# Optimization experiments

Measured on AMD Instinct MI355X. Metric: run time of the kernel, lower is better.

## Reference

```python
import jax, jax.numpy as jnp
import numpy as np

H, DK, NHID, L, G = 8, 32, 256, 2, 16
SQRT_DK = float(np.sqrt(DK))
N_IN = (3, 3, 2)  # number of etypes whose dst is word, topic, doc (for mean cross-reducer)


def _seg_softmax_agg(a, val, dst, n):
    # per-destination-node softmax over incoming edges (DGL mailbox softmax), then weighted sum
    m = jax.ops.segment_max(a, dst, num_segments=n)
    m = jnp.where(m < -1e30, 0.0, m)  # empty segments
    ex = jnp.exp(a - m[dst])
    den = jax.ops.segment_sum(ex, dst, num_segments=n)
    w = ex / jnp.maximum(den, 1e-9)[dst]
    return jax.ops.segment_sum(w[..., None] * val, dst, num_segments=n)  # [n,H,DK]


def _forward(word_id, topic_id, g_word, g_topic, g_doc,
             src_ww, dst_ww, src_wd, dst_wd, src_wt, dst_wt, src_td, dst_td, src_tt, dst_tt,
             time_ww, time_wd, time_wt, time_td, y_data,
             word_embeds, topic_embeds, doc_gen, adapt_w, adapt_b,
             time_tab, time_w, time_b,
             kW, kB, qW, qB, vW, vB, aW, aB, skip, ln_g, ln_b,
             pri, attR, msgR, out_w, out_b):
    nd = g_doc.shape[0]
    # initial node features: word via adapt_ws, topic lookup, doc broadcast
    h = [word_embeds[word_id] @ adapt_w + adapt_b,
         topic_embeds[topic_id],
         jnp.tile(doc_gen, (nd, 1))]
    te = lambda t: time_tab[t] @ time_w + time_b  # RelTemporalEncoding: lin(emb(t)) -> [E, DK]
    th_ww, th_wd, th_wt, th_td = te(time_ww), te(time_wd), te(time_wt), te(time_td)
    # etype index order: wt, wd, td, tt, ww, tw, dt, dw ; ntype index: 0=word,1=topic,2=doc
    rels = [(0, 0, 1, src_wt, dst_wt, th_wt), (1, 0, 2, src_wd, dst_wd, th_wd),
            (2, 1, 2, src_td, dst_td, th_td), (3, 1, 1, src_tt, dst_tt, None),
            (4, 0, 0, src_ww, dst_ww, th_ww), (5, 1, 0, dst_wt, src_wt, th_wt),
            (6, 2, 1, dst_td, src_td, th_td), (7, 2, 0, dst_wd, src_wd, th_wd)]
    for li in range(L):
        k = [(h[i] @ kW[li, i] + kB[li, i]).reshape(-1, H, DK) for i in range(3)]
        q = [(h[i] @ qW[li, i] + qB[li, i]).reshape(-1, H, DK) for i in range(3)]
        v = [(h[i] @ vW[li, i] + vB[li, i]).reshape(-1, H, DK) for i in range(3)]
        t = [jnp.zeros((h[i].shape[0], NHID), h[i].dtype) for i in range(3)]
        for (e, s, d, src, dst, th) in rels:
            key = jnp.einsum('ehk,hkl->ehl', k[s][src], attR[li, e])
            a = (q[d][dst] * key).sum(-1) * pri[li, e] / SQRT_DK  # [E,H]
            val = jnp.einsum('ehk,hkl->ehl', v[s][src], msgR[li, e])
            if th is not None:
                val = val + th[:, None, :]  # temporal encoding broadcast over heads
            n = h[d].shape[0]
            he = _seg_softmax_agg(a, val, dst, n)
            t[d] = t[d] + jax.nn.relu(he.reshape(n, NHID))  # relu per etype, then mean
        nh = []
        for i in range(3):
            alpha = jax.nn.sigmoid(skip[li, i])
            trans = (t[i] / N_IN[i]) @ aW[li, i] + aB[li, i]
            out = trans * alpha + h[i] * (1.0 - alpha)
            mu = out.mean(-1, keepdims=True)
            var = ((out - mu) ** 2).mean(-1, keepdims=True)
            nh.append((out - mu) / jnp.sqrt(var + 1e-5) * ln_g[li, i] + ln_b[li, i])
        h = nh
    gmax = lambda x, g: jax.ops.segment_max(x, g, num_segments=G)  # dgl.max_nodes
    gi = jnp.concatenate([gmax(h[2], g_doc), gmax(h[0], g_word), gmax(h[1], g_topic)], -1)
    logits = gi @ out_w + out_b  # [G,1]
    z = logits.reshape(-1)
    loss = jnp.mean(jnp.maximum(z, 0.0) - z * y_data + jnp.log1p(jnp.exp(-jnp.abs(z))))
    return loss, jax.nn.sigmoid(logits)


def setup_inputs():
    key = jax.random.key(0)
    ks = iter(jax.random.split(key, 80))
    nrm = lambda shape, s=0.05: jax.random.normal(next(ks), shape, jnp.float32) * s
    ri = lambda shape, hi: jax.random.randint(next(ks), shape, 0, hi)
    NW, NT, ND = 30000, 2000, 8000
    d = {}
    d['word_id'] = ri((NW,), 15000)
    d['topic_id'] = ri((NT,), 50)
    d['g_word'] = jnp.sort(ri((NW,), G))
    d['g_topic'] = jnp.sort(ri((NT,), G))
    d['g_doc'] = jnp.sort(ri((ND,), G))
    d['src_ww'] = ri((40000,), NW); d['dst_ww'] = ri((40000,), NW); d['time_ww'] = ri((40000,), 7)
    d['src_wd'] = ri((30000,), NW); d['dst_wd'] = ri((30000,), ND); d['time_wd'] = ri((30000,), 7)
    d['src_wt'] = ri((30000,), NW); d['dst_wt'] = ri((30000,), NT); d['time_wt'] = ri((30000,), 7)
    d['src_td'] = ri((25000,), NT); d['dst_td'] = ri((25000,), ND); d['time_td'] = ri((25000,), 7)
    d['src_tt'] = ri((20000,), NT); d['dst_tt'] = ri((20000,), NT)
    d['y_data'] = jax.random.uniform(next(ks), (G,), jnp.float32)
    d['word_embeds'] = nrm((15000, 256))
    d['topic_embeds'] = nrm((50, 256), 0.1)
    d['doc_gen'] = nrm((1, 256), 0.1)
    d['adapt_w'] = nrm((256, 256)); d['adapt_b'] = nrm((256,), 0.01)
    d['time_tab'] = nrm((7, 32), 0.1); d['time_w'] = nrm((32, 32), 0.1); d['time_b'] = nrm((32,), 0.01)
    for nm in ['kW', 'qW', 'vW', 'aW']:
        d[nm] = nrm((L, 3, 256, 256))
    for nm in ['kB', 'qB', 'vB', 'aB']:
        d[nm] = nrm((L, 3, 256), 0.01)
    d['skip'] = jnp.ones((L, 3))
    d['ln_g'] = jnp.ones((L, 3, 256)); d['ln_b'] = jnp.zeros((L, 3, 256))
    d['pri'] = jnp.ones((L, 8, H))
    d['attR'] = nrm((L, 8, H, DK, DK), 0.1)
    d['msgR'] = nrm((L, 8, H, DK, DK), 0.1)
    d['out_w'] = nrm((3 * NHID, 1)); d['out_b'] = jnp.zeros((1,))
    return d


def reference(word_id, topic_id, g_word, g_topic, g_doc,
              src_ww, dst_ww, time_ww, src_wd, dst_wd, time_wd,
              src_wt, dst_wt, time_wt, src_td, dst_td, time_td,
              src_tt, dst_tt, y_data,
              word_embeds, topic_embeds, doc_gen, adapt_w, adapt_b,
              time_tab, time_w, time_b,
              kW, kB, qW, qB, vW, vB, aW, aB, skip, ln_g, ln_b,
              pri, attR, msgR, out_w, out_b):
    return _forward(word_id, topic_id, g_word, g_topic, g_doc,
                    src_ww, dst_ww, src_wd, dst_wd, src_wt, dst_wt, src_td, dst_td, src_tt, dst_tt,
                    time_ww, time_wd, time_wt, time_td, y_data,
                    word_embeds, topic_embeds, doc_gen, adapt_w, adapt_b,
                    time_tab, time_w, time_b,
                    kW, kB, qW, qB, vW, vB, aW, aB, skip, ln_g, ln_b,
                    pri, attR, msgR, out_w, out_b)
```

## Files before the change

kernel.cpp:

```cpp
#include <hip/hip_runtime.h>
#include <hip/hip_bf16.h>
#include <math.h>

#define H 8
#define DK 32
#define NHID 256
#define LNUM 2
#define GNUM 16

typedef float f32x4 __attribute__((ext_vector_type(4)));
typedef short bf16x8 __attribute__((ext_vector_type(8)));
typedef unsigned short u16x8 __attribute__((ext_vector_type(8)));

__device__ __forceinline__ unsigned encf(float f) {
    unsigned u = __float_as_uint(f);
    return (u & 0x80000000u) ? ~u : (u | 0x80000000u);
}
__device__ __forceinline__ float decf(unsigned u) {
    return __uint_as_float((u & 0x80000000u) ? (u ^ 0x80000000u) : ~u);
}
__device__ __forceinline__ float bfd(unsigned short u) {
    return __uint_as_float(((unsigned)u) << 16);
}
__device__ __forceinline__ unsigned short f2bf(float x) {
    __hip_bfloat16 b = __float2bfloat16(x);
    return *reinterpret_cast<unsigned short*>(&b);
}

#define APAN2(row, kb) ((((kb) >> 7) << 12) + ((row) << 6) + ((((kb) & 127) ^ (((row) & 7) << 4)) >> 1))
__device__ __forceinline__ size_t swzA(int row, int col ) {
    return (((size_t)(row >> 6)) << 14) + (size_t)APAN2(row & 63, col * 2);
}
#define SWZB(row, kb)  (((row) << 6) + ((((kb) ^ (((row) & 7) << 4))) >> 1))

struct CsrArgs { const int* dst[8]; int relOfs[9]; int dstBase[8]; };
struct BdArgs  { const unsigned short* inK[3]; const unsigned short* inV[3];
                 const float* RA[3]; const float* RM[3]; const float* priP[3];
                 int rows[3]; int rowOfs[3]; };
struct Ek1Args { const int* src[3]; const int* dst[3]; int E[3]; int eBase[3]; int rowOfs[3]; };
struct Ek3Args { const int* src[3]; const int* tim[3]; int eBase[3]; int dstBase[3];
                 int rowOfs[3]; int nr; int nD; };
struct GmaxArgs{ const float* hp[3]; const int* grp[3]; int n[3]; int colBase[3]; };
struct GBArgs  { int rb[4]; int nLoc[3]; int li3; };
struct MLArgs  { int rowOfs[4]; int nLoc[3]; int li3; };

__global__ void te_kernel(const float* __restrict__ time_tab, const float* __restrict__ time_w,
                          const float* __restrict__ time_b, float* __restrict__ te7) {
    int t = threadIdx.x >> 5, j = threadIdx.x & 31;
    if (t < 7) {
        float s = time_b[j];
        #pragma unroll
        for (int i = 0; i < 32; ++i) s += time_tab[t * 32 + i] * time_w[i * 32 + j];
        te7[t * 32 + j] = s;
    }
}

__global__ void gather_rows(const float* __restrict__ emb, const int* __restrict__ idx,
                            float* __restrict__ out, unsigned short* __restrict__ outB, int n) {
    int row = blockIdx.x, c = threadIdx.x;
    if (row < n) {
        float v = emb[(size_t)idx[row] * 256 + c];
        out[(size_t)row * 256 + c] = v;
        outB[swzA(row, c)] = f2bf(v);
    }
}

__global__ void bcast_row(const float* __restrict__ src, float* __restrict__ out,
                          unsigned short* __restrict__ outB, int n) {
    int row = blockIdx.x, c = threadIdx.x;
    if (row < n) {
        float v = src[c];
        out[(size_t)row * 256 + c] = v;
        outB[swzA(row, c)] = f2bf(v);
    }
}

__global__ __launch_bounds__(256) void wtr_kernel(
    const float* __restrict__ adaptW, const float* __restrict__ kW, const float* __restrict__ qW,
    const float* __restrict__ vW, const float* __restrict__ aW, unsigned short* __restrict__ WT) {
    int z = blockIdx.z;
    const float* src;
    if (z == 0) src = adaptW;
    else if (z < 7)  src = kW + (size_t)(z - 1) * 65536;
    else if (z < 13) src = qW + (size_t)(z - 7) * 65536;
    else if (z < 19) src = vW + (size_t)(z - 13) * 65536;
    else             src = aW + (size_t)(z - 19) * 65536;
    unsigned short* dst = WT + (size_t)z * 65536;
    __shared__ float tile[32][33];
    int tx = threadIdx.x & 31, ty = threadIdx.x >> 5;
    int kb = blockIdx.x * 32, cb = blockIdx.y * 32;
    #pragma unroll
    for (int i = 0; i < 4; ++i)
        tile[ty + i * 8][tx] = src[(size_t)(kb + ty + i * 8) * 256 + cb + tx];
    __syncthreads();
    #pragma unroll
    for (int i = 0; i < 4; ++i)
        dst[(size_t)(cb + ty + i * 8) * 256 + kb + tx] = f2bf(tile[tx][ty + i * 8]);
}

__global__ __launch_bounds__(256) void gemm_batch(
    const unsigned short* __restrict__ Apan,
    const unsigned short* __restrict__ WT, int wBase, int nz,
    const float* __restrict__ b0, const float* __restrict__ b1, const float* __restrict__ b2,
    void* __restrict__ o0, void* __restrict__ o1, void* __restrict__ o2,
    int outBf16, GBArgs ga)
{
    __shared__ unsigned short As[64 * 256];
    __shared__ unsigned short Bs[2][64 * 64];
    const int tid = threadIdx.x;
    const int lane = tid & 63, wv = tid >> 6;
    const int b = blockIdx.x;
    const int t = (b >= ga.rb[2]) ? 2 : ((b >= ga.rb[1]) ? 1 : 0);
    const int nLoc = ga.nLoc[t];
    const int locRowBase = (b - ga.rb[t]) * 64;
    const int cb = blockIdx.y * 64;
    const int mBase = wBase + ga.li3 + t;
    {
        const u16x8* src = reinterpret_cast<const u16x8*>(Apan + (((size_t)b) << 14));
        u16x8* dst = reinterpret_cast<u16x8*>(As);
        #pragma unroll
        for (int it = 0; it < 8; ++it)
            dst[it * 256 + tid] = src[it * 256 + tid];
    }
    const int fr = lane & 15, fg = lane >> 4;
    const int wrow = (wv & 1) * 32, wcol = (wv >> 1) * 32;
    const int bcol = tid >> 2, bseg = tid & 3;
    const int nt = nz * 4;
    {
        const unsigned short* bsrc = WT + (size_t)mBase * 65536 + (size_t)(cb + bcol) * 256 + bseg * 16;
        u16x8 w0 = *reinterpret_cast<const u16x8*>(bsrc);
        u16x8 w1 = *reinterpret_cast<const u16x8*>(bsrc + 8);
        *reinterpret_cast<u16x8*>(&Bs[0][SWZB(bcol, bseg * 32)])      = w0;
        *reinterpret_cast<u16x8*>(&Bs[0][SWZB(bcol, bseg * 32 + 16)]) = w1;
    }
    __syncthreads();

    f32x4 acc[2][2];
    #pragma unroll
    for (int m = 0; m < 2; ++m)
        #pragma unroll
        for (int nn = 0; nn < 2; ++nn) acc[m][nn] = 0.f;

    for (int tt2 = 0; tt2 < nt; ++tt2) {
        const int cur = tt2 & 1;
        const int ks = tt2 & 3, z = tt2 >> 2;
        u16x8 w0, w1;
        const bool pf = (tt2 + 1 < nt);
        if (pf) {
            int tn = tt2 + 1;
            const unsigned short* bsrc = WT + (size_t)(mBase + (tn >> 2) * 6) * 65536
                                            + (size_t)(cb + bcol) * 256 + (tn & 3) * 64 + bseg * 16;
            w0 = *reinterpret_cast<const u16x8*>(bsrc);
            w1 = *reinterpret_cast<const u16x8*>(bsrc + 8);
        }
        #pragma unroll
        for (int kk = 0; kk < 2; ++kk) {
            bf16x8 af0 = *reinterpret_cast<bf16x8*>(&As[APAN2(wrow + fr,      ks * 128 + kk * 64 + fg * 16)]);
            bf16x8 af1 = *reinterpret_cast<bf16x8*>(&As[APAN2(wrow + 16 + fr, ks * 128 + kk * 64 + fg * 16)]);
            bf16x8 bf0 = *reinterpret_cast<bf16x8*>(&Bs[cur][SWZB(wcol + fr,      kk * 64 + fg * 16)]);
            bf16x8 bf1 = *reinterpret_cast<bf16x8*>(&Bs[cur][SWZB(wcol + 16 + fr, kk * 64 + fg * 16)]);
            acc[0][0] = __builtin_amdgcn_mfma_f32_16x16x32_bf16(af0, bf0, acc[0][0], 0, 0, 0);
            acc[0][1] = __builtin_amdgcn_mfma_f32_16x16x32_bf16(af0, bf1, acc[0][1], 0, 0, 0);
            acc[1][0] = __builtin_amdgcn_mfma_f32_16x16x32_bf16(af1, bf0, acc[1][0], 0, 0, 0);
            acc[1][1] = __builtin_amdgcn_mfma_f32_16x16x32_bf16(af1, bf1, acc[1][1], 0, 0, 0);
        }
        if (pf) {
            *reinterpret_cast<u16x8*>(&Bs[cur ^ 1][SWZB(bcol, bseg * 32)])      = w0;
            *reinterpret_cast<u16x8*>(&Bs[cur ^ 1][SWZB(bcol, bseg * 32 + 16)]) = w1;
        }
        if (ks == 3) {
            const float* biasB = (z == 0) ? b0 : ((z == 1) ? b1 : b2);
            const float* bias = biasB + (size_t)(ga.li3 + t) * 256;
            void* outp = (z == 0) ? o0 : ((z == 1) ? o1 : o2);
            #pragma unroll
            for (int m = 0; m < 2; ++m) {
                #pragma unroll
                for (int r = 0; r < 4; ++r) {
                    int lr = locRowBase + wrow + m * 16 + fg * 4 + r;
                    if (lr >= nLoc) continue;
                    size_t gr = (size_t)b * 64 + wrow + m * 16 + fg * 4 + r;
                    #pragma unroll
                    for (int nn = 0; nn < 2; ++nn) {
                        int gc = cb + wcol + nn * 16 + fr;
                        float v = acc[m][nn][r] + bias[gc];
                        if (outBf16) ((unsigned short*)outp)[gr * 256 + gc] = f2bf(v);
                        else         ((float*)outp)[gr * 256 + gc] = v;
                    }
                }
            }
            #pragma unroll
            for (int m = 0; m < 2; ++m)
                #pragma unroll
                for (int nn = 0; nn < 2; ++nn) acc[m][nn] = 0.f;
        }
        __syncthreads();
    }
}

__global__ __launch_bounds__(256) void gemm_init(
    const float* __restrict__ A, const int* __restrict__ gidx,
    const unsigned short* __restrict__ WT, const float* __restrict__ bias,
    float* __restrict__ outF, unsigned short* __restrict__ dupB, int n)
{
    __shared__ unsigned short As[64 * 256];
    __shared__ unsigned short Bs[2][64 * 64];
    const int tid = threadIdx.x;
    const int lane = tid & 63, wv = tid >> 6;
    const int rowBase = blockIdx.x * 64;
    const int cb = blockIdx.y * 64;
    #pragma unroll 4
    for (int it = 0; it < 16; ++it) {
        int row = it * 4 + wv;
        int r = rowBase + row;
        ushort4 p = make_ushort4(0, 0, 0, 0);
        if (r < n) {
            int ar = gidx[r];
            float4 v = *reinterpret_cast<const float4*>(A + (size_t)ar * 256 + lane * 4);
            p.x = f2bf(v.x); p.y = f2bf(v.y); p.z = f2bf(v.z); p.w = f2bf(v.w);
        }
        *reinterpret_cast<ushort4*>(&As[APAN2(row, lane * 8)]) = p;
    }
    const int fr = lane & 15, fg = lane >> 4;
    const int wrow = (wv & 1) * 32, wcol = (wv >> 1) * 32;
    const int bcol = tid >> 2, bseg = tid & 3;
    {
        const unsigned short* bsrc = WT + (size_t)(cb + bcol) * 256 + bseg * 16;
        u16x8 w0 = *reinterpret_cast<const u16x8*>(bsrc);
        u16x8 w1 = *reinterpret_cast<const u16x8*>(bsrc + 8);
        *reinterpret_cast<u16x8*>(&Bs[0][SWZB(bcol, bseg * 32)])      = w0;
        *reinterpret_cast<u16x8*>(&Bs[0][SWZB(bcol, bseg * 32 + 16)]) = w1;
    }
    __syncthreads();
    f32x4 acc[2][2];
    #pragma unroll
    for (int m = 0; m < 2; ++m)
        #pragma unroll
        for (int nn = 0; nn < 2; ++nn) acc[m][nn] = 0.f;
    for (int t = 0; t < 4; ++t) {
        const int cur = t & 1;
        u16x8 w0, w1;
        const bool pf = (t + 1 < 4);
        if (pf) {
            const unsigned short* bsrc = WT + (size_t)(cb + bcol) * 256 + (t + 1) * 64 + bseg * 16;
            w0 = *reinterpret_cast<const u16x8*>(bsrc);
            w1 = *reinterpret_cast<const u16x8*>(bsrc + 8);
        }
        #pragma unroll
        for (int kk = 0; kk < 2; ++kk) {
            bf16x8 af0 = *reinterpret_cast<bf16x8*>(&As[APAN2(wrow + fr,      t * 128 + kk * 64 + fg * 16)]);
            bf16x8 af1 = *reinterpret_cast<bf16x8*>(&As[APAN2(wrow + 16 + fr, t * 128 + kk * 64 + fg * 16)]);
            bf16x8 bf0 = *reinterpret_cast<bf16x8*>(&Bs[cur][SWZB(wcol + fr,      kk * 64 + fg * 16)]);
            bf16x8 bf1 = *reinterpret_cast<bf16x8*>(&Bs[cur][SWZB(wcol + 16 + fr, kk * 64 + fg * 16)]);
            acc[0][0] = __builtin_amdgcn_mfma_f32_16x16x32_bf16(af0, bf0, acc[0][0], 0, 0, 0);
            acc[0][1] = __builtin_amdgcn_mfma_f32_16x16x32_bf16(af0, bf1, acc[0][1], 0, 0, 0);
            acc[1][0] = __builtin_amdgcn_mfma_f32_16x16x32_bf16(af1, bf0, acc[1][0], 0, 0, 0);
            acc[1][1] = __builtin_amdgcn_mfma_f32_16x16x32_bf16(af1, bf1, acc[1][1], 0, 0, 0);
        }
        if (pf) {
            *reinterpret_cast<u16x8*>(&Bs[cur ^ 1][SWZB(bcol, bseg * 32)])      = w0;
            *reinterpret_cast<u16x8*>(&Bs[cur ^ 1][SWZB(bcol, bseg * 32 + 16)]) = w1;
        }
        __syncthreads();
    }
    #pragma unroll
    for (int m = 0; m < 2; ++m) {
        #pragma unroll
        for (int r = 0; r < 4; ++r) {
            int gr = rowBase + wrow + m * 16 + fg * 4 + r;
            if (gr >= n) continue;
            #pragma unroll
            for (int nn = 0; nn < 2; ++nn) {
                int gc = cb + wcol + nn * 16 + fr;
                float v = acc[m][nn][r] + bias[gc];
                outF[(size_t)gr * 256 + gc] = v;
                dupB[swzA(gr, gc)] = f2bf(v);
            }
        }
    }
}

__global__ __launch_bounds__(256) void bd_mfma(
    unsigned short* __restrict__ katt, unsigned short* __restrict__ vmsg, BdArgs A)
{
    const int rr = blockIdx.z >> 1, isV = blockIdx.z & 1;
    const int n = A.rows[rr];
    const int rowBase = blockIdx.x * 128;
    if (rowBase >= n) return;
    const unsigned short* in = isV ? A.inV[rr] : A.inK[rr];
    const float* R = isV ? A.RM[rr] : A.RA[rr];
    unsigned short* out = (isV ? vmsg : katt) + (size_t)A.rowOfs[rr] * 256;
    const int head = blockIdx.y;
    const float oscale = isV ? 1.f : (A.priP[rr][head] * 0.17677669529663687f);
    const int tid = threadIdx.x, lane = tid & 63, wv = tid >> 6;
    const int fr = lane & 15, fg = lane >> 4;
    const float* Rh = R + head * 1024;
    bf16x8 b0, b1;
    #pragma unroll
    for (int j = 0; j < 8; ++j) {
        b0[j] = (short)f2bf(Rh[(fg * 8 + j) * 32 + fr] * oscale);
        b1[j] = (short)f2bf(Rh[(fg * 8 + j) * 32 + 16 + fr] * oscale);
    }
    const int r0 = rowBase + wv * 32 + fr;
    const int r1 = r0 + 16;
    const int rc0 = (r0 < n) ? r0 : n - 1;
    const int rc1 = (r1 < n) ? r1 : n - 1;
    bf16x8 a0 = *reinterpret_cast<const bf16x8*>(in + (size_t)rc0 * 256 + head * 32 + fg * 8);
    bf16x8 a1 = *reinterpret_cast<const bf16x8*>(in + (size_t)rc1 * 256 + head * 32 + fg * 8);
    f32x4 acc00 = 0.f, acc01 = 0.f, acc10 = 0.f, acc11 = 0.f;
    acc00 = __builtin_amdgcn_mfma_f32_16x16x32_bf16(a0, b0, acc00, 0, 0, 0);
    acc01 = __builtin_amdgcn_mfma_f32_16x16x32_bf16(a0, b1, acc01, 0, 0, 0);
    acc10 = __builtin_amdgcn_mfma_f32_16x16x32_bf16(a1, b0, acc10, 0, 0, 0);
    acc11 = __builtin_amdgcn_mfma_f32_16x16x32_bf16(a1, b1, acc11, 0, 0, 0);
    const int colB = head * 32 + fr;
    #pragma unroll
    for (int r = 0; r < 4; ++r) {
        int g0 = rowBase + wv * 32 + fg * 4 + r;
        if (g0 < n) {
            out[(size_t)g0 * 256 + colB]      = f2bf(acc00[r]);
            out[(size_t)g0 * 256 + colB + 16] = f2bf(acc01[r]);
        }
        int g1 = g0 + 16;
        if (g1 < n) {
            out[(size_t)g1 * 256 + colB]      = f2bf(acc10[r]);
            out[(size_t)g1 * 256 + colB + 16] = f2bf(acc11[r]);
        }
    }
}

__global__ __launch_bounds__(256) void ek1_group(
    const unsigned short* __restrict__ qbuf, const unsigned short* __restrict__ katt,
    float* __restrict__ alog, Ek1Args A)
{
    const int rr = blockIdx.y;
    int gid = blockIdx.x * 256 + threadIdx.x;
    int e = gid >> 3, h = gid & 7;
    if (e >= A.E[rr]) return;
    int s = A.src[rr][e], d = A.dst[rr][e];
    const u16x8* q8 = reinterpret_cast<const u16x8*>(qbuf + (size_t)d * 256 + h * 32);
    const u16x8* k8 = reinterpret_cast<const u16x8*>(katt + ((size_t)(A.rowOfs[rr] + s)) * 256 + h * 32);
    float a = 0.f;
    #pragma unroll
    for (int j = 0; j < 4; ++j) {
        u16x8 qv = q8[j], kv = k8[j];
        #pragma unroll
        for (int m = 0; m < 8; ++m) a += bfd(qv[m]) * bfd(kv[m]);
    }
    alog[(size_t)(A.eBase[rr] + e) * 8 + h] = a;
}

__global__ __launch_bounds__(256) void ek3_group(
    const unsigned short* __restrict__ vmsg, const float* __restrict__ alog,
    const int* __restrict__ rowptrAll, const int* __restrict__ eidxAll,
    const float* __restrict__ te7, unsigned short* __restrict__ tacc, float outScale, Ek3Args A)
{
    __shared__ float sTe[224];
    if (threadIdx.x < 224) sTe[threadIdx.x] = te7[threadIdx.x];
    __syncthreads();
    int wv = threadIdx.x >> 6, lane = threadIdx.x & 63;
    int d = blockIdx.x * 4 + wv;
    if (d >= A.nD) return;
    const int bl = lane >> 3, hl = lane & 7;
    const int c = lane * 4, hq = lane >> 3;
    float t0 = 0.f, t1 = 0.f, t2 = 0.f, t3 = 0.f;
    for (int rr = 0; rr < A.nr; ++rr) {
        int base = A.dstBase[rr] + d;
        int beg = rowptrAll[base], end = rowptrAll[base + 1];
        if (beg == end) continue;
        const int* srcp = A.src[rr];
        const int* timp = A.tim[rr];
        int eB = A.eBase[rr], rO = A.rowOfs[rr];
        float m = -INFINITY, den = 0.f;
        float a0 = 0.f, a1 = 0.f, a2 = 0.f, a3 = 0.f;
        for (int p0 = beg; p0 < end; p0 += 8) {
            int p = p0 + bl;
            bool valid = p < end;
            int ge = eidxAll[valid ? p : end - 1];
            int le = ge - eB;
            float a = valid ? alog[(size_t)ge * 8 + hl] : -INFINITY;
            int sS = valid ? srcp[le] : 0;
            int tT = (timp && valid) ? timp[le] : 0;
            float bm = a;
            bm = fmaxf(bm, __shfl_xor(bm, 8));
            bm = fmaxf(bm, __shfl_xor(bm, 16));
            bm = fmaxf(bm, __shfl_xor(bm, 32));
            float bmA = __shfl(bm, hq);
            float mN = fmaxf(m, bmA);
            float sc = __expf(m - mN);
            den *= sc; a0 *= sc; a1 *= sc; a2 *= sc; a3 *= sc;
            m = mN;
            float mL = __shfl(mN, hl * 8);
            float ex = valid ? __expf(a - mL) : 0.f;
            float ds = ex;
            ds += __shfl_xor(ds, 8);
            ds += __shfl_xor(ds, 16);
            ds += __shfl_xor(ds, 32);
            den += __shfl(ds, hq);
            int nb = end - p0; if (nb > 8) nb = 8;
            for (int b = 0; b < nb; ++b) {
                float w = __shfl(ex, b * 8 + hq);
                int sB = __shfl(sS, b * 8);
                ushort4 v = *reinterpret_cast<const ushort4*>(vmsg + ((size_t)(rO + sB)) * 256 + c);
                float vx = bfd(v.x), vy = bfd(v.y), vz = bfd(v.z), vw = bfd(v.w);
                if (timp) {
                    int tB = __shfl(tT, b * 8);
                    const float* tp = &sTe[tB * 32 + (c & 31)];
                    vx += tp[0]; vy += tp[1]; vz += tp[2]; vw += tp[3];
                }
                a0 += w * vx; a1 += w * vy; a2 += w * vz; a3 += w * vw;
            }
        }
        float inv = 1.f / fmaxf(den, 1e-9f);
        t0 += fmaxf(a0 * inv, 0.f); t1 += fmaxf(a1 * inv, 0.f);
        t2 += fmaxf(a2 * inv, 0.f); t3 += fmaxf(a3 * inv, 0.f);
    }
    ushort4 o;
    o.x = f2bf(t0 * outScale); o.y = f2bf(t1 * outScale);
    o.z = f2bf(t2 * outScale); o.w = f2bf(t3 * outScale);
    *reinterpret_cast<ushort4*>(tacc + swzA(d, c)) = o;
}

__global__ void count_all(CsrArgs A, int* __restrict__ cnt, int totE) {
    int gid = blockIdx.x * 256 + threadIdx.x;
    if (gid >= totE) return;
    int r = 0;
    while (gid >= A.relOfs[r + 1]) ++r;
    int e = gid - A.relOfs[r];
    atomicAdd(&cnt[A.dstBase[r] + A.dst[r][e]], 1);
}
__global__ __launch_bounds__(1024) void scan1_k(const int* __restrict__ cnt, int* __restrict__ part,
                                                int* __restrict__ bsum, int n) {
    __shared__ int buf[1024];
    int tid = threadIdx.x, gid = blockIdx.x * 1024 + tid;
    int x = (gid < n) ? cnt[gid] : 0;
    buf[tid] = x; __syncthreads();
    for (int off = 1; off < 1024; off <<= 1) {
        int y = (tid >= off) ? buf[tid - off] : 0;
        __syncthreads();
        buf[tid] += y;
        __syncthreads();
    }
    if (gid < n) part[gid] = buf[tid];
    if (tid == 1023) bsum[blockIdx.x] = buf[1023];
}
__global__ __launch_bounds__(256) void scan2_k(int* __restrict__ bsum, int nb) {
    __shared__ int buf[256];
    int tid = threadIdx.x;
    buf[tid] = (tid < nb) ? bsum[tid] : 0;
    __syncthreads();
    for (int off = 1; off < 256; off <<= 1) {
        int y = (tid >= off) ? buf[tid - off] : 0;
        __syncthreads();
        buf[tid] += y;
        __syncthreads();
    }
    if (tid < nb) bsum[tid] = buf[tid];
}
__global__ void scan3_k(const int* __restrict__ cnt, const int* __restrict__ part,
                        const int* __restrict__ bsum, int* __restrict__ rowptr,
                        int* __restrict__ cur, int n) {
    int gid = blockIdx.x * 256 + threadIdx.x;
    if (gid < n) {
        int b = gid >> 10;
        int add = (b > 0) ? bsum[b - 1] : 0;
        int inc = part[gid] + add;
        rowptr[gid + 1] = inc;
        cur[gid] = inc - cnt[gid];
    }
    if (gid == 0) rowptr[0] = 0;
}
__global__ void scatter_all(CsrArgs A, int* __restrict__ cur, int* __restrict__ eidx, int totE) {
    int gid = blockIdx.x * 256 + threadIdx.x;
    if (gid >= totE) return;
    int r = 0;
    while (gid >= A.relOfs[r + 1]) ++r;
    int e = gid - A.relOfs[r];
    int p = atomicAdd(&cur[A.dstBase[r] + A.dst[r][e]], 1);
    eidx[p] = gid;
}

__global__ __launch_bounds__(256) void mix_ln_all(
    float* __restrict__ h, unsigned short* __restrict__ hB, const float* __restrict__ trans,
    const float* __restrict__ skipP, const float* __restrict__ g, const float* __restrict__ b,
    MLArgs M)
{
    int row = blockIdx.x;
    int t = (row >= M.rowOfs[2]) ? 2 : ((row >= M.rowOfs[1]) ? 1 : 0);
    int d = row - M.rowOfs[t];
    if (d >= M.nLoc[t]) return;
    int j = M.li3 + t;
    int c = threadIdx.x;
    float alpha = 1.f / (1.f + expf(-skipP[j]));
    size_t off = (size_t)row * 256 + c;
    float o = trans[off] * alpha + h[off] * (1.f - alpha);
    float s = o, ss = o * o;
    #pragma unroll
    for (int dd = 1; dd < 64; dd <<= 1) { s += __shfl_xor(s, dd); ss += __shfl_xor(ss, dd); }
    __shared__ float rS[4], rSS[4];
    int w = threadIdx.x >> 6, lane = threadIdx.x & 63;
    if (lane == 0) { rS[w] = s; rSS[w] = ss; }
    __syncthreads();
    float S = rS[0] + rS[1] + rS[2] + rS[3];
    float SS = rSS[0] + rSS[1] + rSS[2] + rSS[3];
    float mean = S * (1.f / 256.f);
    float var = fmaxf(SS * (1.f / 256.f) - mean * mean, 0.f);
    float rs = rsqrtf(var + 1e-5f);
    float v = (o - mean) * rs * g[(size_t)j * 256 + c] + b[(size_t)j * 256 + c];
    h[off] = v;
    hB[swzA(row, c)] = f2bf(v);
}

__global__ __launch_bounds__(256) void gmax_all(GmaxArgs A, unsigned* __restrict__ gi) {
    int ty = blockIdx.y;
    int n = A.n[ty];
    int r0 = blockIdx.x * 64;
    if (r0 >= n) return;
    int col = threadIdx.x;
    const float* hp = A.hp[ty];
    const int* grp = A.grp[ty];
    int cbase = A.colBase[ty];
    int rend = (r0 + 64 < n) ? r0 + 64 : n;
    int cur = grp[r0];
    float m = -INFINITY;
    for (int r = r0; r < rend; ++r) {
        int g = grp[r];
        if (g != cur) {
            atomicMax(&gi[cur * 768 + cbase + col], encf(m));
            cur = g; m = -INFINITY;
        }
        m = fmaxf(m, hp[(size_t)r * 256 + col]);
    }
    atomicMax(&gi[cur * 768 + cbase + col], encf(m));
}

__global__ void gi_init(unsigned* __restrict__ gi) {
    int i = blockIdx.x * 256 + threadIdx.x;
    if (i < 16 * 768) gi[i] = 0x007FFFFFu;
}

__global__ __launch_bounds__(1024) void final_k(const unsigned* __restrict__ gi,
                                                const float* __restrict__ out_w,
                                                const float* __restrict__ out_b,
                                                const float* __restrict__ y,
                                                float* __restrict__ out) {
    int w = threadIdx.x >> 6, lane = threadIdx.x & 63;
    float s = 0.f;
    for (int c = lane; c < 768; c += 64) s += decf(gi[w * 768 + c]) * out_w[c];
    #pragma unroll
    for (int d = 1; d < 64; d <<= 1) s += __shfl_xor(s, d);
    __shared__ float lloss[16];
    if (lane == 0) {
        float z = s + out_b[0];
        out[1 + w] = 1.f / (1.f + expf(-z));
        lloss[w] = fmaxf(z, 0.f) - z * y[w] + log1pf(expf(-fabsf(z)));
    }
    __syncthreads();
    if (threadIdx.x == 0) {
        float L = 0.f;
        for (int g2 = 0; g2 < 16; ++g2) L += lloss[g2];
        out[0] = L * (1.f / 16.f);
    }
}

extern "C" void kernel_launch(void* const* d_in, const int* in_sizes, int n_in,
                              void* d_out, int out_size, void* d_ws, size_t ws_size,
                              hipStream_t stream) {
    const int* word_id   = (const int*)d_in[0];
    const int* topic_id  = (const int*)d_in[1];
    const int* g_word    = (const int*)d_in[2];
    const int* g_topic   = (const int*)d_in[3];
    const int* g_doc     = (const int*)d_in[4];
    const int* src_ww = (const int*)d_in[5];  const int* dst_ww = (const int*)d_in[6];  const int* time_ww = (const int*)d_in[7];
    const int* src_wd = (const int*)d_in[8];  const int* dst_wd = (const int*)d_in[9];  const int* time_wd = (const int*)d_in[10];
    const int* src_wt = (const int*)d_in[11]; const int* dst_wt = (const int*)d_in[12]; const int* time_wt = (const int*)d_in[13];
    const int* src_td = (const int*)d_in[14]; const int* dst_td = (const int*)d_in[15]; const int* time_td = (const int*)d_in[16];
    const int* src_tt = (const int*)d_in[17]; const int* dst_tt = (const int*)d_in[18];
    const float* y_data      = (const float*)d_in[19];
    const float* word_embeds = (const float*)d_in[20];
    const float* topic_embeds= (const float*)d_in[21];
    const float* doc_gen     = (const float*)d_in[22];
    const float* adapt_w     = (const float*)d_in[23];
    const float* adapt_b     = (const float*)d_in[24];
    const float* time_tab    = (const float*)d_in[25];
    const float* time_w      = (const float*)d_in[26];
    const float* time_b      = (const float*)d_in[27];
    const float* kW = (const float*)d_in[28];
    const float* qW = (const float*)d_in[29];
    const float* vW = (const float*)d_in[30];
    const float* aW = (const float*)d_in[31];
    const float* kB = (const float*)d_in[32];
    const float* qB = (const float*)d_in[33];
    const float* vB = (const float*)d_in[34];
    const float* aB = (const float*)d_in[35];
    const float* skip = (const float*)d_in[36];
    const float* ln_g = (const float*)d_in[37];
    const float* ln_b = (const float*)d_in[38];
    const float* pri  = (const float*)d_in[39];
    const float* attR = (const float*)d_in[40];
    const float* msgR = (const float*)d_in[41];
    const float* out_w = (const float*)d_in[42];
    const float* out_b = (const float*)d_in[43];

    const int NW = in_sizes[0], NT = in_sizes[1], ND = in_sizes[4];
    const int E_ww = in_sizes[5], E_wd = in_sizes[8], E_wt = in_sizes[11],
              E_td = in_sizes[14], E_tt = in_sizes[17];
    const int nN[3] = {NW, NT, ND};
    const float invNin[3] = {1.f / 3.f, 1.f / 3.f, 1.f / 2.f};

    struct Rel { int e, s, d; const int* src; const int* dst; const int* tim; int E; };
    const Rel rels[8] = {
        {0, 0, 1, src_wt, dst_wt, time_wt, E_wt},
        {1, 0, 2, src_wd, dst_wd, time_wd, E_wd},
        {2, 1, 2, src_td, dst_td, time_td, E_td},
        {3, 1, 1, src_tt, dst_tt, nullptr, E_tt},
        {4, 0, 0, src_ww, dst_ww, time_ww, E_ww},
        {5, 1, 0, dst_wt, src_wt, time_wt, E_wt},
        {6, 2, 1, dst_td, src_td, time_td, E_td},
        {7, 2, 0, dst_wd, src_wd, time_wd, E_wd},
    };

    int relOfs[9]; relOfs[0] = 0;
    int dstBase[8]; int acc = 0;
    for (int r = 0; r < 8; ++r) { relOfs[r + 1] = relOfs[r] + rels[r].E; dstBase[r] = acc; acc += nN[rels[r].d]; }
    const int totE = relOfs[8], totD = acc;

    const int grpRels[3][3] = {{4, 5, 7}, {0, 3, 6}, {1, 2, 0}};
    const int nrG[3] = {3, 3, 2};
    int rowOfsG[3][3], grpRows[3];
    for (int g = 0; g < 3; ++g) {
        int ro = 0;
        for (int j = 0; j < nrG[g]; ++j) { rowOfsG[g][j] = ro; ro += nN[rels[grpRels[g][j]].s]; }
        grpRows[g] = ro;
    }
    int maxGrpRows = 0;
    for (int g = 0; g < 3; ++g) if (grpRows[g] > maxGrpRows) maxGrpRows = grpRows[g];

    int nPad[3], rowOfsT[4];
    rowOfsT[0] = 0;
    for (int i = 0; i < 3; ++i) { nPad[i] = (nN[i] + 63) & ~63; rowOfsT[i + 1] = rowOfsT[i] + nPad[i]; }
    const int totPad = rowOfsT[3];

    float* base = (float*)d_ws;
    size_t off = 0;
    auto take = [&](size_t nElems) { float* p = base + off; off += (nElems + 63) & ~(size_t)63; return p; };
    float* hPbase = take((size_t)totPad * 256);
    unsigned short* hB = (unsigned short*)take((size_t)totPad * 128);
    unsigned short* tB = (unsigned short*)take((size_t)totPad * 128);
    unsigned short* kPb = (unsigned short*)take((size_t)totPad * 128);
    unsigned short* qPb = (unsigned short*)take((size_t)totPad * 128);
    unsigned short* vPb = (unsigned short*)take((size_t)totPad * 128);
    size_t uniFloats = (size_t)maxGrpRows * 256;
    if ((size_t)totPad * 256 > uniFloats) uniFloats = (size_t)totPad * 256;
    float* uni = take(uniFloats);
    unsigned short* kattB = (unsigned short*)uni;
    unsigned short* vmsgB = (unsigned short*)(uni + (size_t)maxGrpRows * 128);
    float* trans = uni;
    unsigned short* WT = (unsigned short*)take((size_t)25 * 32768);
    float* alog = take((size_t)totE * 8);
    float* te7  = take(7 * 32);
    unsigned* gi = (unsigned*)take(16 * 768);
    int* cntAll = (int*)take(totD);
    int* part   = (int*)take(totD);
    int* bsum   = (int*)take(256);
    int* rowptrAll = (int*)take(totD + 1);
    int* curAll = (int*)take(totD);
    int* eidxAll = (int*)take(totE);
    (void)ws_size; (void)n_in; (void)out_size;

    te_kernel<<<1, 256, 0, stream>>>(time_tab, time_w, time_b, te7);
    {
        dim3 g(8, 8, 25);
        wtr_kernel<<<g, 256, 0, stream>>>(adapt_w, kW, qW, vW, aW, WT);
    }
    CsrArgs ca;
    for (int r = 0; r < 8; ++r) { ca.dst[r] = rels[r].dst; ca.dstBase[r] = dstBase[r]; }
    for (int r = 0; r < 9; ++r) ca.relOfs[r] = relOfs[r];
    hipMemsetAsync(cntAll, 0, (size_t)totD * sizeof(int), stream);
    count_all<<<(totE + 255) / 256, 256, 0, stream>>>(ca, cntAll, totE);
    int nb = (totD + 1023) / 1024;
    scan1_k<<<nb, 1024, 0, stream>>>(cntAll, part, bsum, totD);
    scan2_k<<<1, 256, 0, stream>>>(bsum, nb);
    scan3_k<<<(totD + 255) / 256, 256, 0, stream>>>(cntAll, part, bsum, rowptrAll, curAll, totD);
    scatter_all<<<(totE + 255) / 256, 256, 0, stream>>>(ca, curAll, eidxAll, totE);
    gi_init<<<48, 256, 0, stream>>>(gi);

    {
        dim3 g((NW + 63) / 64, 4);
        gemm_init<<<g, 256, 0, stream>>>(word_embeds, word_id, WT, adapt_b, hPbase, hB, NW);
    }
    gather_rows<<<NT, 256, 0, stream>>>(topic_embeds, topic_id,
                                        hPbase + (size_t)rowOfsT[1] * 256,
                                        hB + (size_t)rowOfsT[1] * 256, NT);
    bcast_row<<<ND, 256, 0, stream>>>(doc_gen,
                                      hPbase + (size_t)rowOfsT[2] * 256,
                                      hB + (size_t)rowOfsT[2] * 256, ND);

    Ek1Args e1a[3]; Ek3Args e3a[3];
    int maxE_g[3];
    for (int g = 0; g < 3; ++g) {
        int me = 0;
        for (int j = 0; j < 3; ++j) {
            int jr = (j < nrG[g]) ? grpRels[g][j] : grpRels[g][0];
            const Rel& R = rels[jr];
            e1a[g].src[j] = R.src; e1a[g].dst[j] = R.dst;
            e1a[g].E[j] = (j < nrG[g]) ? R.E : 0;
            e1a[g].eBase[j] = relOfs[jr];
            e1a[g].rowOfs[j] = (j < nrG[g]) ? rowOfsG[g][j] : 0;
            e3a[g].src[j] = R.src; e3a[g].tim[j] = R.tim;
            e3a[g].eBase[j] = relOfs[jr]; e3a[g].dstBase[j] = dstBase[jr];
            e3a[g].rowOfs[j] = (j < nrG[g]) ? rowOfsG[g][j] : 0;
            if (j < nrG[g] && R.E > me) me = R.E;
        }
        e3a[g].nr = nrG[g]; e3a[g].nD = nN[g];
        maxE_g[g] = me;
    }

    GBArgs gb;
    for (int i = 0; i < 4; ++i) gb.rb[i] = rowOfsT[i] / 64;
    for (int i = 0; i < 3; ++i) gb.nLoc[i] = nN[i];
    MLArgs ml;
    for (int i = 0; i < 4; ++i) ml.rowOfs[i] = rowOfsT[i];
    for (int i = 0; i < 3; ++i) ml.nLoc[i] = nN[i];

    const int totBlocks = totPad / 64;
    for (int li = 0; li < LNUM; ++li) {
        gb.li3 = li * 3; ml.li3 = li * 3;
        {
            dim3 g(totBlocks, 4);
            gemm_batch<<<g, 256, 0, stream>>>(hB, WT, 1, 3, kB, qB, vB,
                                              kPb, qPb, vPb, 1, gb);
        }
        for (int g = 0; g < 3; ++g) {
            BdArgs ba;
            int maxRows = 0;
            for (int j = 0; j < 3; ++j) {
                int jr = (j < nrG[g]) ? grpRels[g][j] : grpRels[g][0];
                const Rel& R = rels[jr];
                ba.inK[j] = kPb + (size_t)rowOfsT[R.s] * 256;
                ba.inV[j] = vPb + (size_t)rowOfsT[R.s] * 256;
                ba.RA[j] = attR + ((size_t)li * 8 + R.e) * 8192;
                ba.RM[j] = msgR + ((size_t)li * 8 + R.e) * 8192;
                ba.priP[j] = pri + ((size_t)li * 8 + R.e) * 8;
                ba.rows[j] = (j < nrG[g]) ? nN[R.s] : 0;
                ba.rowOfs[j] = (j < nrG[g]) ? rowOfsG[g][j] : 0;
                if (ba.rows[j] > maxRows) maxRows = ba.rows[j];
            }
            dim3 gbd((maxRows + 127) / 128, 8, 2 * nrG[g]);
            bd_mfma<<<gbd, 256, 0, stream>>>(kattB, vmsgB, ba);
            dim3 g1((maxE_g[g] * 8 + 255) / 256, nrG[g]);
            ek1_group<<<g1, 256, 0, stream>>>(qPb + (size_t)rowOfsT[g] * 256, kattB, alog, e1a[g]);
            ek3_group<<<(nN[g] + 3) / 4, 256, 0, stream>>>(vmsgB, alog, rowptrAll, eidxAll,
                                                           te7, tB + (size_t)rowOfsT[g] * 256,
                                                           invNin[g], e3a[g]);
        }
        {
            dim3 g(totBlocks, 4);
            gemm_batch<<<g, 256, 0, stream>>>(tB, WT, 19, 1, aB, aB, aB,
                                              trans, trans, trans, 0, gb);
        }
        mix_ln_all<<<totPad, 256, 0, stream>>>(hPbase, hB, trans, skip, ln_g, ln_b, ml);
    }

    GmaxArgs ga;
    ga.hp[0] = hPbase + (size_t)rowOfsT[2] * 256; ga.grp[0] = g_doc;   ga.n[0] = ND; ga.colBase[0] = 0;
    ga.hp[1] = hPbase;                             ga.grp[1] = g_word;  ga.n[1] = NW; ga.colBase[1] = 256;
    ga.hp[2] = hPbase + (size_t)rowOfsT[1] * 256; ga.grp[2] = g_topic; ga.n[2] = NT; ga.colBase[2] = 512;
    int maxN = NW > ND ? (NW > NT ? NW : NT) : (ND > NT ? ND : NT);
    dim3 gg((maxN + 63) / 64, 3);
    gmax_all<<<gg, 256, 0, stream>>>(ga, gi);
    final_k<<<1, 1024, 0, stream>>>(gi, out_w, out_b, y_data, (float*)d_out);
}
```

Before: 723.0 us.

## Pre-swizzle weight tiles and widen gemm_batch to 128-column tiles

The weight transpose kernel now writes bf16 weights directly in the swizzled 64x64 tile layout used in LDS. gemm_batch and gemm_init can then fill shared memory with plain contiguous vector copies instead of per-thread swizzled scatter. gemm_batch also doubles its output tile width to 128 columns, with each wave holding 2x4 MFMA accumulators. This halves the grid's y dimension and reuses each A panel load across twice as many columns. The cost is more LDS per block (larger B buffers), more registers, and fewer blocks for the fixed-size GEMMs.

Result: slower. 739.4 us (+2.3%).

```diff
diff --git a/kernel.cpp b/kernel.cpp
--- a/kernel.cpp
+++ b/kernel.cpp
@@ -94,8 +94,11 @@
         tile[ty + i * 8][tx] = src[(size_t)(kb + ty + i * 8) * 256 + cb + tx];
     __syncthreads();
     #pragma unroll
-    for (int i = 0; i < 4; ++i)
-        dst[(size_t)(cb + ty + i * 8) * 256 + kb + tx] = f2bf(tile[tx][ty + i * 8]);
+    for (int i = 0; i < 4; ++i) {
+        int col = cb + ty + i * 8, k = kb + tx;
+        dst[((col >> 6) * 4 + (k >> 6)) * 4096 + SWZB(col & 63, (k & 63) * 2)] =
+            f2bf(tile[tx][ty + i * 8]);
+    }
 }
 
 __global__ __launch_bounds__(256) void gemm_batch(
@@ -106,14 +109,14 @@
     int outBf16, GBArgs ga)
 {
     __shared__ unsigned short As[64 * 256];
-    __shared__ unsigned short Bs[2][64 * 64];
+    __shared__ unsigned short Bs[2][8192];
     const int tid = threadIdx.x;
     const int lane = tid & 63, wv = tid >> 6;
     const int b = blockIdx.x;
     const int t = (b >= ga.rb[2]) ? 2 : ((b >= ga.rb[1]) ? 1 : 0);
     const int nLoc = ga.nLoc[t];
     const int locRowBase = (b - ga.rb[t]) * 64;
-    const int cb = blockIdx.y * 64;
+    const int cb2 = blockIdx.y;
     const int mBase = wBase + ga.li3 + t;
     {
         const u16x8* src = reinterpret_cast<const u16x8*>(Apan + (((size_t)b) << 14));
@@ -123,50 +126,61 @@
             dst[it * 256 + tid] = src[it * 256 + tid];
     }
     const int fr = lane & 15, fg = lane >> 4;
-    const int wrow = (wv & 1) * 32, wcol = (wv >> 1) * 32;
-    const int bcol = tid >> 2, bseg = tid & 3;
+    const int wrow = (wv & 1) * 32, cc = wv >> 1;
     const int nt = nz * 4;
     {
-        const unsigned short* bsrc = WT + (size_t)mBase * 65536 + (size_t)(cb + bcol) * 256 + bseg * 16;
-        u16x8 w0 = *reinterpret_cast<const u16x8*>(bsrc);
-        u16x8 w1 = *reinterpret_cast<const u16x8*>(bsrc + 8);
-        *reinterpret_cast<u16x8*>(&Bs[0][SWZB(bcol, bseg * 32)])      = w0;
-        *reinterpret_cast<u16x8*>(&Bs[0][SWZB(bcol, bseg * 32 + 16)]) = w1;
+        const unsigned short* base0 = WT + (size_t)mBase * 65536;
+        u16x8* dst = reinterpret_cast<u16x8*>(Bs[0]);
+        #pragma unroll
+        for (int j2 = 0; j2 < 4; ++j2) {
+            int e = tid + j2 * 256;
+            int ch = e >> 9, eo = e & 511;
+            dst[e] = *reinterpret_cast<const u16x8*>(base0 + ((cb2 * 2 + ch) * 4 + 0) * 4096 + eo * 8);
+        }
     }
     __syncthreads();
 
-    f32x4 acc[2][2];
+    f32x4 acc[2][4];
     #pragma unroll
     for (int m = 0; m < 2; ++m)
         #pragma unroll
-        for (int nn = 0; nn < 2; ++nn) acc[m][nn] = 0.f;
+        for (int nn = 0; nn < 4; ++nn) acc[m][nn] = 0.f;
 
     for (int tt2 = 0; tt2 < nt; ++tt2) {
         const int cur = tt2 & 1;
         const int ks = tt2 & 3, z = tt2 >> 2;
-        u16x8 w0, w1;
+        u16x8 w[4];
         const bool pf = (tt2 + 1 < nt);
         if (pf) {
             int tn = tt2 + 1;
-            const unsigned short* bsrc = WT + (size_t)(mBase + (tn >> 2) * 6) * 65536
-                                            + (size_t)(cb + bcol) * 256 + (tn & 3) * 64 + bseg * 16;
-            w0 = *reinterpret_cast<const u16x8*>(bsrc);
-            w1 = *reinterpret_cast<const u16x8*>(bsrc + 8);
+            const unsigned short* baseN = WT + (size_t)(mBase + (tn >> 2) * 6) * 65536;
+            int ksN = tn & 3;
+            #pragma unroll
+            for (int j2 = 0; j2 < 4; ++j2) {
+                int e = tid + j2 * 256;
+                int ch = e >> 9, eo = e & 511;
+                w[j2] = *reinterpret_cast<const u16x8*>(baseN + ((cb2 * 2 + ch) * 4 + ksN) * 4096 + eo * 8);
+            }
         }
         #pragma unroll
         for (int kk = 0; kk < 2; ++kk) {
             bf16x8 af0 = *reinterpret_cast<bf16x8*>(&As[APAN2(wrow + fr,      ks * 128 + kk * 64 + fg * 16)]);
             bf16x8 af1 = *reinterpret_cast<bf16x8*>(&As[APAN2(wrow + 16 + fr, ks * 128 + kk * 64 + fg * 16)]);
-            bf16x8 bf0 = *reinterpret_cast<bf16x8*>(&Bs[cur][SWZB(wcol + fr,      kk * 64 + fg * 16)]);
-            bf16x8 bf1 = *reinterpret_cast<bf16x8*>(&Bs[cur][SWZB(wcol + 16 + fr, kk * 64 + fg * 16)]);
-            acc[0][0] = __builtin_amdgcn_mfma_f32_16x16x32_bf16(af0, bf0, acc[0][0], 0, 0, 0);
-            acc[0][1] = __builtin_amdgcn_mfma_f32_16x16x32_bf16(af0, bf1, acc[0][1], 0, 0, 0);
-            acc[1][0] = __builtin_amdgcn_mfma_f32_16x16x32_bf16(af1, bf0, acc[1][0], 0, 0, 0);
-            acc[1][1] = __builtin_amdgcn_mfma_f32_16x16x32_bf16(af1, bf1, acc[1][1], 0, 0, 0);
+            bf16x8 bf[4];
+            #pragma unroll
+            for (int nn = 0; nn < 4; ++nn)
+                bf[nn] = *reinterpret_cast<bf16x8*>(&Bs[cur][cc * 4096 + SWZB(nn * 16 + fr, kk * 64 + fg * 16)]);
+            #pragma unroll
+            for (int nn = 0; nn < 4; ++nn) {
+                acc[0][nn] = __builtin_amdgcn_mfma_f32_16x16x32_bf16(af0, bf[nn], acc[0][nn], 0, 0, 0);
+                acc[1][nn] = __builtin_amdgcn_mfma_f32_16x16x32_bf16(af1, bf[nn], acc[1][nn], 0, 0, 0);
+            }
         }
         if (pf) {
-            *reinterpret_cast<u16x8*>(&Bs[cur ^ 1][SWZB(bcol, bseg * 32)])      = w0;
-            *reinterpret_cast<u16x8*>(&Bs[cur ^ 1][SWZB(bcol, bseg * 32 + 16)]) = w1;
+            u16x8* dst = reinterpret_cast<u16x8*>(Bs[cur ^ 1]);
+            #pragma unroll
+            for (int j2 = 0; j2 < 4; ++j2)
+                dst[tid + j2 * 256] = w[j2];
         }
         if (ks == 3) {
             const float* biasB = (z == 0) ? b0 : ((z == 1) ? b1 : b2);
@@ -180,8 +194,8 @@
                     if (lr >= nLoc) continue;
                     size_t gr = (size_t)b * 64 + wrow + m * 16 + fg * 4 + r;
                     #pragma unroll
-                    for (int nn = 0; nn < 2; ++nn) {
-                        int gc = cb + wcol + nn * 16 + fr;
+                    for (int nn = 0; nn < 4; ++nn) {
+                        int gc = cb2 * 128 + cc * 64 + nn * 16 + fr;
                         float v = acc[m][nn][r] + bias[gc];
                         if (outBf16) ((unsigned short*)outp)[gr * 256 + gc] = f2bf(v);
                         else         ((float*)outp)[gr * 256 + gc] = v;
@@ -191,7 +205,7 @@
             #pragma unroll
             for (int m = 0; m < 2; ++m)
                 #pragma unroll
-                for (int nn = 0; nn < 2; ++nn) acc[m][nn] = 0.f;
+                for (int nn = 0; nn < 4; ++nn) acc[m][nn] = 0.f;
         }
         __syncthreads();
     }
@@ -203,11 +217,11 @@
     float* __restrict__ outF, unsigned short* __restrict__ dupB, int n)
 {
     __shared__ unsigned short As[64 * 256];
-    __shared__ unsigned short Bs[2][64 * 64];
+    __shared__ unsigned short Bs[2][4096];
     const int tid = threadIdx.x;
     const int lane = tid & 63, wv = tid >> 6;
     const int rowBase = blockIdx.x * 64;
-    const int cb = blockIdx.y * 64;
+    const int cb6 = blockIdx.y;
     #pragma unroll 4
     for (int it = 0; it < 16; ++it) {
         int row = it * 4 + wv;
@@ -222,13 +236,13 @@
     }
     const int fr = lane & 15, fg = lane >> 4;
     const int wrow = (wv & 1) * 32, wcol = (wv >> 1) * 32;
-    const int bcol = tid >> 2, bseg = tid & 3;
     {
-        const unsigned short* bsrc = WT + (size_t)(cb + bcol) * 256 + bseg * 16;
-        u16x8 w0 = *reinterpret_cast<const u16x8*>(bsrc);
-        u16x8 w1 = *reinterpret_cast<const u16x8*>(bsrc + 8);
-        *reinterpret_cast<u16x8*>(&Bs[0][SWZB(bcol, bseg * 32)])      = w0;
-        *reinterpret_cast<u16x8*>(&Bs[0][SWZB(bcol, bseg * 32 + 16)]) = w1;
+        u16x8* dst = reinterpret_cast<u16x8*>(Bs[0]);
+        #pragma unroll
+        for (int j2 = 0; j2 < 2; ++j2) {
+            int e = tid + j2 * 256;
+            dst[e] = *reinterpret_cast<const u16x8*>(WT + (cb6 * 4 + 0) * 4096 + e * 8);
+        }
     }
     __syncthreads();
     f32x4 acc[2][2];
@@ -238,12 +252,14 @@
         for (int nn = 0; nn < 2; ++nn) acc[m][nn] = 0.f;
     for (int t = 0; t < 4; ++t) {
         const int cur = t & 1;
-        u16x8 w0, w1;
+        u16x8 w[2];
         const bool pf = (t + 1 < 4);
         if (pf) {
-            const unsigned short* bsrc = WT + (size_t)(cb + bcol) * 256 + (t + 1) * 64 + bseg * 16;
-            w0 = *reinterpret_cast<const u16x8*>(bsrc);
-            w1 = *reinterpret_cast<const u16x8*>(bsrc + 8);
+            #pragma unroll
+            for (int j2 = 0; j2 < 2; ++j2) {
+                int e = tid + j2 * 256;
+                w[j2] = *reinterpret_cast<const u16x8*>(WT + (cb6 * 4 + t + 1) * 4096 + e * 8);
+            }
         }
         #pragma unroll
         for (int kk = 0; kk < 2; ++kk) {
@@ -257,8 +273,10 @@
             acc[1][1] = __builtin_amdgcn_mfma_f32_16x16x32_bf16(af1, bf1, acc[1][1], 0, 0, 0);
         }
         if (pf) {
-            *reinterpret_cast<u16x8*>(&Bs[cur ^ 1][SWZB(bcol, bseg * 32)])      = w0;
-            *reinterpret_cast<u16x8*>(&Bs[cur ^ 1][SWZB(bcol, bseg * 32 + 16)]) = w1;
+            u16x8* dst = reinterpret_cast<u16x8*>(Bs[cur ^ 1]);
+            #pragma unroll
+            for (int j2 = 0; j2 < 2; ++j2)
+                dst[tid + j2 * 256] = w[j2];
         }
         __syncthreads();
     }
@@ -270,7 +288,7 @@
             if (gr >= n) continue;
             #pragma unroll
             for (int nn = 0; nn < 2; ++nn) {
-                int gc = cb + wcol + nn * 16 + fr;
+                int gc = cb6 * 64 + wcol + nn * 16 + fr;
                 float v = acc[m][nn][r] + bias[gc];
                 outF[(size_t)gr * 256 + gc] = v;
                 dupB[swzA(gr, gc)] = f2bf(v);
@@ -725,7 +743,7 @@
     for (int li = 0; li < LNUM; ++li) {
         gb.li3 = li * 3; ml.li3 = li * 3;
         {
-            dim3 g(totBlocks, 4);
+            dim3 g(totBlocks, 2);
             gemm_batch<<<g, 256, 0, stream>>>(hB, WT, 1, 3, kB, qB, vB,
                                               kPb, qPb, vPb, 1, gb);
         }
@@ -753,7 +771,7 @@
                                                            invNin[g], e3a[g]);
         }
         {
-            dim3 g(totBlocks, 4);
+            dim3 g(totBlocks, 2);
             gemm_batch<<<g, 256, 0, stream>>>(tB, WT, 19, 1, aB, aB, aB,
                                               trans, trans, trans, 0, gb);
         }
```
